# Kernel tuning notes

Hardware: AMD Instinct MI355X
Metric: run time of the kernel (lower is better)

The kernel has to match this reference:

```python
import jax, jax.numpy as jnp
import numpy as np

MASK_VALUE = -10000000.0


def setup_inputs() -> dict:
    key = jax.random.key(0)
    ks = jax.random.split(key, 8)
    U, I, J, C, E = 128, 256, 512, 128, 128
    return {
        "target_items_context": jax.random.normal(ks[0], (U, I, C), jnp.float32),
        "interacted_items_context": jax.random.normal(ks[1], (U, J, C), jnp.float32),
        "user_embeds": jax.random.normal(ks[2], (U, E), jnp.float32),
        "attention_mask": jax.random.randint(ks[3], (U, J), 0, 2) > 0,
        "w_dense": jax.random.normal(ks[4], (2 * C,), jnp.float32) * 0.02,
        "b_dense": jax.random.normal(ks[5], (1,), jnp.float32) * 0.02,
        "W_mlp": jax.random.normal(ks[6], (E + C, C), jnp.float32) * 0.02,
        "b_mlp": jax.random.normal(ks[7], (C,), jnp.float32) * 0.02,
    }


def reference(target_items_context, interacted_items_context, user_embeds,
              attention_mask, w_dense, b_dense, W_mlp, b_mlp):
    C = target_items_context.shape[-1]
    E = user_embeds.shape[-1]
    # additive attention score: tanh([t; k] @ w + b) = tanh(t@w1 + k@w2 + b)
    # (dropout is identity in eval mode)
    s_t = jnp.einsum('uic,c->ui', target_items_context, w_dense[:C])      # (U, I)
    s_k = jnp.einsum('ujc,c->uj', interacted_items_context, w_dense[C:])  # (U, J)
    scores = jnp.tanh(s_t[:, :, None] + s_k[:, None, :] + b_dense[0])     # (U, I, J)
    scores = scores + (~attention_mask)[:, None, :].astype(scores.dtype) * MASK_VALUE
    attn = jax.nn.softmax(scores, axis=-1)                                # (U, I, J)
    # weighted pooling of interacted contexts
    pooled = jnp.einsum('uij,ujc->uic', attn, interacted_items_context)   # (U, I, C)
    # mlp: relu([user; pooled] @ W + b) = relu(user@W[:E] + pooled@W[E:] + b)
    u_part = user_embeds @ W_mlp[:E]                                      # (U, C)
    user_context = jax.nn.relu(u_part[:, None, :] + pooled @ W_mlp[E:] + b_mlp)
    return user_context, attn
```

## Files before the change

kernel.cpp:

```cpp
#include <hip/hip_runtime.h>

#define UU 128
#define II 256
#define JJ 512
#define CC 128
#define EE 128
#define IB 16
#define NIB 16
#define JT 64
#define NJT 8
#define VTP 72

typedef short bf16x8 __attribute__((ext_vector_type(8)));
typedef float f32x4 __attribute__((ext_vector_type(4)));

union FragU { bf16x8 v; unsigned u[4]; };

__device__ __forceinline__ float fast_tanh(float x) {
    float ex = __expf(2.0f * x);
    return 1.0f - 2.0f / (ex + 1.0f);
}

__device__ __forceinline__ unsigned pack_bf16x2(float lo, float hi) {
    unsigned ul = __float_as_uint(lo), uh = __float_as_uint(hi);
    ul = (ul + 0x7FFFu + ((ul >> 16) & 1u)) >> 16;
    uh = (uh + 0x7FFFu + ((uh >> 16) & 1u)) >> 16;
    return ul | (uh << 16);
}

__device__ __forceinline__ short bf16s(float f) {
    unsigned u = __float_as_uint(f);
    u = (u + 0x7FFFu + ((u >> 16) & 1u)) >> 16;
    return (short)u;
}

__device__ __forceinline__ float wave_reduce_add(float v) {
#pragma unroll
    for (int k = 32; k >= 1; k >>= 1) v += __shfl_xor(v, k, 64);
    return v;
}

#define VT_BLOCKS (UU * NJT)
#define UP_BLOCKS (UU * CC / 256)

__global__ void precompute_kernel(const float* __restrict__ itc,
                                  const float* __restrict__ user,
                                  const float* __restrict__ wd,
                                  const float* __restrict__ Wm,
                                  const float* __restrict__ bm,
                                  float* __restrict__ sk_g,
                                  float* __restrict__ up_g,
                                  short* __restrict__ vtg,
                                  short* __restrict__ wtg) {
    __shared__ float vt_f[JT][CC + 4];
    int b = blockIdx.x;
    int t = threadIdx.x;
    if (b < VT_BLOCKS) {
        int u = b & 127, jt = b >> 7;
        const float* src = itc + ((size_t)u * JJ + jt * JT) * CC;
#pragma unroll
        for (int k = 0; k < 8; ++k) {
            int f = t + 256 * k;
            int row = f >> 5, c4 = (f & 31) * 4;
            *(float4*)&vt_f[row][c4] = *(const float4*)&src[(size_t)row * CC + c4];
        }
        __syncthreads();
        {
            int r = t >> 2, q4 = t & 3;
            float s = 0.f;
#pragma unroll
            for (int cc = 0; cc < 32; cc += 4) {
                float4 a = *(const float4*)&vt_f[r][q4 * 32 + cc];
                float4 w = *(const float4*)&wd[CC + q4 * 32 + cc];
                s += a.x * w.x + a.y * w.y + a.z * w.z + a.w * w.w;
            }
            s += __shfl_xor(s, 1, 64);
            s += __shfl_xor(s, 2, 64);
            if (q4 == 0) sk_g[u * JJ + jt * JT + r] = s;
        }
        {
            int c = t & 127, half = t >> 7;
            unsigned* dst = (unsigned*)(vtg + (size_t)(u * NJT + jt) * 8192) +
                            half * 2048 + c * 16;
#pragma unroll
            for (int m = 0; m < 16; ++m) {
                dst[m] = pack_bf16x2(vt_f[32 * half + 2 * m][c],
                                     vt_f[32 * half + 2 * m + 1][c]);
            }
        }
    } else if (b < VT_BLOCKS + UP_BLOCKS) {
        int idx = (b - VT_BLOCKS) * 256 + t;
        int u = idx >> 7, c = idx & 127;
        float acc = bm[c];
#pragma unroll 8
        for (int e = 0; e < EE; ++e) acc += user[u * EE + e] * Wm[e * CC + c];
        up_g[idx] = acc;
    } else {
        int n = t & 127, khalf = t >> 7;
#pragma unroll
        for (int ks2 = 0; ks2 < 2; ++ks2) {
            int ks = khalf * 2 + ks2;
#pragma unroll
            for (int g = 0; g < 4; ++g) {
                unsigned q[4];
#pragma unroll
                for (int pr = 0; pr < 4; ++pr) {
                    float lo = Wm[(size_t)(EE + 32 * ks + 8 * g + 2 * pr) * CC + n];
                    float hi = Wm[(size_t)(EE + 32 * ks + 8 * g + 2 * pr + 1) * CC + n];
                    q[pr] = pack_bf16x2(lo, hi);
                }
                *(uint4*)&wtg[ks * 4096 + n * 32 + 8 * g] =
                    make_uint4(q[0], q[1], q[2], q[3]);
            }
        }
    }
}

__global__ __launch_bounds__(256, 4) void fused_main(
    const float* __restrict__ tgt, const int* __restrict__ mask,
    const float* __restrict__ wd, const float* __restrict__ bd,
    const float* __restrict__ sk_g, const float* __restrict__ up_g,
    const short* __restrict__ vt_g, const short* __restrict__ wt_g,
    float* __restrict__ out_ctx, float* __restrict__ out_attn) {
    __shared__ __align__(16) short ps[8192];
    __shared__ __align__(16) short pooled_bf[2048];
    __shared__ float dinv_lds[IB];

    int b = blockIdx.x;
    int x = b & 7, qq = b >> 3;
    int u = x + 8 * (qq >> 4);
    int ib = qq & 15;
    int i0 = ib * IB;
    int t = threadIdx.x;
    int w = t >> 6, l = t & 63, ln = l & 15, g = l >> 4;
    int r = t >> 4, s4 = t & 15;

    float sv;
    {
        const float* trow = tgt + ((size_t)(u * II + i0 + r)) * CC + s4 * 8;
        float4 t0 = *(const float4*)&trow[0];
        float4 t1 = *(const float4*)&trow[4];
        float4 w0 = *(const float4*)&wd[s4 * 8];
        float4 w1 = *(const float4*)&wd[s4 * 8 + 4];
        float part = t0.x * w0.x + t0.y * w0.y + t0.z * w0.z + t0.w * w0.w +
                     t1.x * w1.x + t1.y * w1.y + t1.z * w1.z + t1.w * w1.w;
        part += __shfl_xor(part, 1, 64);
        part += __shfl_xor(part, 2, 64);
        part += __shfl_xor(part, 4, 64);
        part += __shfl_xor(part, 8, 64);
        sv = part + bd[0];
    }

    const float* skb = sk_g + u * JJ;
    const int* mkb = mask + u * JJ;
    unsigned pk[16];
    float rowsum = 0.f;
#pragma unroll
    for (int h = 0; h < 4; ++h) {
        int jb = 8 * (s4 + 16 * h);
        float4 k0 = *(const float4*)&skb[jb];
        float4 k1 = *(const float4*)&skb[jb + 4];
        int4 m0 = *(const int4*)&mkb[jb];
        int4 m1 = *(const int4*)&mkb[jb + 4];
        float p0 = m0.x ? __expf(fast_tanh(sv + k0.x)) : 0.f;
        float p1 = m0.y ? __expf(fast_tanh(sv + k0.y)) : 0.f;
        float p2 = m0.z ? __expf(fast_tanh(sv + k0.z)) : 0.f;
        float p3 = m0.w ? __expf(fast_tanh(sv + k0.w)) : 0.f;
        float p4 = m1.x ? __expf(fast_tanh(sv + k1.x)) : 0.f;
        float p5 = m1.y ? __expf(fast_tanh(sv + k1.y)) : 0.f;
        float p6 = m1.z ? __expf(fast_tanh(sv + k1.z)) : 0.f;
        float p7 = m1.w ? __expf(fast_tanh(sv + k1.w)) : 0.f;
        rowsum += p0 + p1 + p2 + p3 + p4 + p5 + p6 + p7;
        unsigned q0 = pack_bf16x2(p0, p1);
        unsigned q1 = pack_bf16x2(p2, p3);
        unsigned q2 = pack_bf16x2(p4, p5);
        unsigned q3 = pack_bf16x2(p6, p7);
        pk[4 * h + 0] = q0; pk[4 * h + 1] = q1;
        pk[4 * h + 2] = q2; pk[4 * h + 3] = q3;
        int gp = (s4 + 16 * h) ^ (r & 7);
        *(uint4*)((char*)ps + r * 1024 + 16 * gp) = make_uint4(q0, q1, q2, q3);
    }
    rowsum += __shfl_xor(rowsum, 1, 64);
    rowsum += __shfl_xor(rowsum, 2, 64);
    rowsum += __shfl_xor(rowsum, 4, 64);
    rowsum += __shfl_xor(rowsum, 8, 64);
    float dinv = 1.0f / rowsum;
    if (s4 == 0) dinv_lds[r] = dinv;

    const short* b_base =
        vt_g + (size_t)u * (NJT * 8192) + (32 * w + ln) * 32 + 8 * g;
    bf16x8 pb0[8], pb1[8];
#pragma unroll
    for (int s = 0; s < 8; ++s) {
        int off = (s >> 1) * 8192 + (s & 1) * 4096;
        pb0[s] = *(const bf16x8*)&b_base[off];
        pb1[s] = *(const bf16x8*)&b_base[off + 512];
    }

    {
        float* ab = out_attn + ((size_t)(u * II + i0 + r)) * JJ;
#pragma unroll
        for (int h = 0; h < 4; ++h) {
            int jb = 8 * (s4 + 16 * h);
            unsigned q0 = pk[4 * h], q1 = pk[4 * h + 1];
            unsigned q2 = pk[4 * h + 2], q3 = pk[4 * h + 3];
            f32x4 v0, v1;
            v0[0] = __uint_as_float(q0 << 16) * dinv;
            v0[1] = __uint_as_float(q0 & 0xFFFF0000u) * dinv;
            v0[2] = __uint_as_float(q1 << 16) * dinv;
            v0[3] = __uint_as_float(q1 & 0xFFFF0000u) * dinv;
            v1[0] = __uint_as_float(q2 << 16) * dinv;
            v1[1] = __uint_as_float(q2 & 0xFFFF0000u) * dinv;
            v1[2] = __uint_as_float(q3 << 16) * dinv;
            v1[3] = __uint_as_float(q3 & 0xFFFF0000u) * dinv;
            __builtin_nontemporal_store(v0, (f32x4*)&ab[jb]);
            __builtin_nontemporal_store(v1, (f32x4*)&ab[jb + 4]);
        }
    }

    asm volatile("s_waitcnt lgkmcnt(0)" ::: "memory");
    __builtin_amdgcn_s_barrier();
    asm volatile("" ::: "memory");

    f32x4 acc0 = {0.f, 0.f, 0.f, 0.f};
    f32x4 acc1 = {0.f, 0.f, 0.f, 0.f};
#pragma unroll
    for (int s = 0; s < 16; ++s) {
        bf16x8 af = *(const bf16x8*)((const char*)ps + ln * 1024 +
                                     16 * ((4 * s + g) ^ (ln & 7)));
        acc0 = __builtin_amdgcn_mfma_f32_16x16x32_bf16(af, pb0[s & 7], acc0, 0, 0, 0);
        acc1 = __builtin_amdgcn_mfma_f32_16x16x32_bf16(af, pb1[s & 7], acc1, 0, 0, 0);
        if (s < 8) {
            int off = ((s + 8) >> 1) * 8192 + ((s + 8) & 1) * 4096;
            pb0[s & 7] = *(const bf16x8*)&b_base[off];
            pb1[s & 7] = *(const bf16x8*)&b_base[off + 512];
        }
    }

    const short* wbase = wt_g + (32 * w + ln) * 32 + 8 * g;
    bf16x8 wb0[4], wb1[4];
#pragma unroll
    for (int ks = 0; ks < 4; ++ks) {
        wb0[ks] = *(const bf16x8*)&wbase[ks * 4096];
        wb1[ks] = *(const bf16x8*)&wbase[ks * 4096 + 512];
    }

#pragma unroll
    for (int ri = 0; ri < 4; ++ri) {
        int row = 4 * g + ri;
        float dv = dinv_lds[row];
        int c0 = 32 * w + ln;
        int by0 = row * 256 + 16 * ((c0 >> 3) ^ (row & 7)) + 2 * (ln & 7);
        *(short*)((char*)pooled_bf + by0) = bf16s(acc0[ri] * dv);
        int c1 = c0 + 16;
        int by1 = row * 256 + 16 * ((c1 >> 3) ^ (row & 7)) + 2 * (ln & 7);
        *(short*)((char*)pooled_bf + by1) = bf16s(acc1[ri] * dv);
    }
    asm volatile("s_waitcnt lgkmcnt(0)" ::: "memory");
    __builtin_amdgcn_s_barrier();
    asm volatile("" ::: "memory");

    f32x4 oa0 = {0.f, 0.f, 0.f, 0.f};
    f32x4 oa1 = {0.f, 0.f, 0.f, 0.f};
#pragma unroll
    for (int ks = 0; ks < 4; ++ks) {
        bf16x8 pa = *(const bf16x8*)((const char*)pooled_bf + ln * 256 +
                                     16 * ((4 * ks + g) ^ (ln & 7)));
        oa0 = __builtin_amdgcn_mfma_f32_16x16x32_bf16(pa, wb0[ks], oa0, 0, 0, 0);
        oa1 = __builtin_amdgcn_mfma_f32_16x16x32_bf16(pa, wb1[ks], oa1, 0, 0, 0);
    }
    {
        int c0 = 32 * w + ln, c1 = c0 + 16;
        float up0v = up_g[u * CC + c0];
        float up1v = up_g[u * CC + c1];
        float* ctx = out_ctx + ((size_t)(u * II + i0)) * CC;
#pragma unroll
        for (int ri = 0; ri < 4; ++ri) {
            int row = 4 * g + ri;
            __builtin_nontemporal_store(fmaxf(oa0[ri] + up0v, 0.f),
                                        &ctx[(size_t)row * CC + c0]);
            __builtin_nontemporal_store(fmaxf(oa1[ri] + up1v, 0.f),
                                        &ctx[(size_t)row * CC + c1]);
        }
    }
}

__global__ __launch_bounds__(256, 3) void fused_fallback(
    const float* __restrict__ tgt, const float* __restrict__ itc,
    const float* __restrict__ user, const int* __restrict__ mask,
    const float* __restrict__ wd, const float* __restrict__ bd,
    const float* __restrict__ Wm, const float* __restrict__ bm,
    float* __restrict__ out_ctx, float* __restrict__ out_attn) {
    __shared__ __align__(16) short Vt[CC][VTP];
    __shared__ __align__(16) float pool[IB][CC + 4];
    __shared__ __align__(16) float skv[JJ];
    __shared__ __align__(16) float stv[IB];
    __shared__ __align__(16) float upv[CC];
    __shared__ __align__(16) float dinv_lds[IB];
    __shared__ unsigned char mk[JJ];

    int b = blockIdx.x;
    int x = b & 7, q = b >> 3;
    int u = x + 8 * (q >> 4);
    int ib = q & 15;
    int i0 = ib * IB;
    int t = threadIdx.x;

    mk[t] = (unsigned char)(mask[u * JJ + t] != 0);
    mk[t + 256] = (unsigned char)(mask[u * JJ + t + 256] != 0);

    {
        int lane = t & 63, w4 = t >> 6;
        float2 w2 = *(const float2*)&wd[CC + lane * 2];
        for (int r = w4; r < JJ; r += 4) {
            float2 a = *(const float2*)&itc[((size_t)u * JJ + r) * CC + lane * 2];
            float s = wave_reduce_add(a.x * w2.x + a.y * w2.y);
            if (lane == 0) skv[r] = s;
        }
        float2 w1 = *(const float2*)&wd[lane * 2];
        float bdv = bd[0];
        for (int r = w4; r < IB; r += 4) {
            float2 a = *(const float2*)&tgt[((size_t)u * II + i0 + r) * CC + lane * 2];
            float s = wave_reduce_add(a.x * w1.x + a.y * w1.y);
            if (lane == 0) stv[r] = s + bdv;
        }
        if (t < CC) {
            float acc = bm[t];
            for (int e = 0; e < EE; ++e) acc += user[u * EE + e] * Wm[e * CC + t];
            upv[t] = acc;
        }
    }
    __syncthreads();

    const int l = t & 63;
    const int w = t >> 6;
    const int ln = l & 15;
    const int g = l >> 4;

    bf16x8 a[16];
    float rowsum = 0.0f;
    {
        float s = stv[ln];
#pragma unroll
        for (int t16 = 0; t16 < 16; ++t16) {
            int j = 32 * t16 + 8 * g;
            float4 k0 = *(const float4*)&skv[j];
            float4 k1 = *(const float4*)&skv[j + 4];
            unsigned m0 = *(const unsigned*)&mk[j];
            unsigned m1 = *(const unsigned*)&mk[j + 4];
            float pf[8];
            pf[0] = (m0 & 0x000000FFu) ? __expf(fast_tanh(s + k0.x)) : 0.0f;
            pf[1] = (m0 & 0x0000FF00u) ? __expf(fast_tanh(s + k0.y)) : 0.0f;
            pf[2] = (m0 & 0x00FF0000u) ? __expf(fast_tanh(s + k0.z)) : 0.0f;
            pf[3] = (m0 & 0xFF000000u) ? __expf(fast_tanh(s + k0.w)) : 0.0f;
            pf[4] = (m1 & 0x000000FFu) ? __expf(fast_tanh(s + k1.x)) : 0.0f;
            pf[5] = (m1 & 0x0000FF00u) ? __expf(fast_tanh(s + k1.y)) : 0.0f;
            pf[6] = (m1 & 0x00FF0000u) ? __expf(fast_tanh(s + k1.z)) : 0.0f;
            pf[7] = (m1 & 0xFF000000u) ? __expf(fast_tanh(s + k1.w)) : 0.0f;
            rowsum += pf[0] + pf[1] + pf[2] + pf[3] + pf[4] + pf[5] + pf[6] + pf[7];
            FragU cu;
            cu.u[0] = pack_bf16x2(pf[0], pf[1]);
            cu.u[1] = pack_bf16x2(pf[2], pf[3]);
            cu.u[2] = pack_bf16x2(pf[4], pf[5]);
            cu.u[3] = pack_bf16x2(pf[6], pf[7]);
            a[t16] = cu.v;
        }
    }
    rowsum += __shfl_xor(rowsum, 16, 64);
    rowsum += __shfl_xor(rowsum, 32, 64);
    float dinv = 1.0f / rowsum;
    if (t < 16) dinv_lds[t] = dinv;

    {
        float* abase = out_attn + ((size_t)(u * II + i0 + ln)) * JJ + 8 * g;
#pragma unroll
        for (int t16 = 0; t16 < 16; ++t16) {
            FragU cu; cu.v = a[t16];
            float f0 = __uint_as_float(cu.u[0] << 16) * dinv;
            float f1 = __uint_as_float(cu.u[0] & 0xFFFF0000u) * dinv;
            float f2 = __uint_as_float(cu.u[1] << 16) * dinv;
            float f3 = __uint_as_float(cu.u[1] & 0xFFFF0000u) * dinv;
            float f4 = __uint_as_float(cu.u[2] << 16) * dinv;
            float f5 = __uint_as_float(cu.u[2] & 0xFFFF0000u) * dinv;
            float f6 = __uint_as_float(cu.u[3] << 16) * dinv;
            float f7 = __uint_as_float(cu.u[3] & 0xFFFF0000u) * dinv;
            *(float4*)&abase[32 * t16] = make_float4(f0, f1, f2, f3);
            *(float4*)&abase[32 * t16 + 4] = make_float4(f4, f5, f6, f7);
        }
    }

    f32x4 acc0 = {0.f, 0.f, 0.f, 0.f};
    f32x4 acc1 = {0.f, 0.f, 0.f, 0.f};
    const float* Vu = itc + (size_t)u * JJ * CC;
    const int cg = t & 31;
    const int jp = t >> 5;
    const int n0 = w * 32;

    for (int jt = 0; jt < 8; ++jt) {
        int j0 = jt * JT;
        __syncthreads();
#pragma unroll
        for (int it = 0; it < 4; ++it) {
            int jl = 2 * (jp + 8 * it);
            const float* r0 = &Vu[(size_t)(j0 + jl) * CC];
            const float* r1 = r0 + CC;
#pragma unroll
            for (int qv = 0; qv < 4; ++qv) {
                int c = cg + 32 * qv;
                *(unsigned*)&Vt[c][jl] = pack_bf16x2(r0[c], r1[c]);
            }
        }
        __syncthreads();
#pragma unroll
        for (int kk = 0; kk < 2; ++kk) {
            bf16x8 b0 = *(const bf16x8*)&Vt[n0 + ln][32 * kk + 8 * g];
            bf16x8 b1 = *(const bf16x8*)&Vt[n0 + 16 + ln][32 * kk + 8 * g];
            acc0 = __builtin_amdgcn_mfma_f32_16x16x32_bf16(a[2 * jt + kk], b0,
                                                           acc0, 0, 0, 0);
            acc1 = __builtin_amdgcn_mfma_f32_16x16x32_bf16(a[2 * jt + kk], b1,
                                                           acc1, 0, 0, 0);
        }
    }

    __syncthreads();
    {
        float4 dv = *(const float4*)&dinv_lds[4 * g];
        float dvr[4] = {dv.x, dv.y, dv.z, dv.w};
#pragma unroll
        for (int r = 0; r < 4; ++r) {
            pool[4 * g + r][n0 + ln] = acc0[r] * dvr[r];
            pool[4 * g + r][n0 + 16 + ln] = acc1[r] * dvr[r];
        }
    }
    __syncthreads();

    {
        int tx = t & 15, ty = t >> 4;
        float o[8];
#pragma unroll
        for (int k = 0; k < 8; ++k) o[k] = 0.f;
#pragma unroll 4
        for (int k = 0; k < CC; ++k) {
            float pk = pool[ty][k];
            float4 w0 = *(const float4*)&Wm[(size_t)(EE + k) * CC + tx * 8];
            float4 w1 = *(const float4*)&Wm[(size_t)(EE + k) * CC + tx * 8 + 4];
            o[0] += pk * w0.x; o[1] += pk * w0.y; o[2] += pk * w0.z; o[3] += pk * w0.w;
            o[4] += pk * w1.x; o[5] += pk * w1.y; o[6] += pk * w1.z; o[7] += pk * w1.w;
        }
        float4 up0 = *(const float4*)&upv[tx * 8];
        float4 up1 = *(const float4*)&upv[tx * 8 + 4];
        float4 r0, r1;
        r0.x = fmaxf(o[0] + up0.x, 0.f); r0.y = fmaxf(o[1] + up0.y, 0.f);
        r0.z = fmaxf(o[2] + up0.z, 0.f); r0.w = fmaxf(o[3] + up0.w, 0.f);
        r1.x = fmaxf(o[4] + up1.x, 0.f); r1.y = fmaxf(o[5] + up1.y, 0.f);
        r1.z = fmaxf(o[6] + up1.z, 0.f); r1.w = fmaxf(o[7] + up1.w, 0.f);
        float* ctx = out_ctx + ((size_t)(u * II + i0 + ty)) * CC + tx * 8;
        *(float4*)&ctx[0] = r0;
        *(float4*)&ctx[4] = r1;
    }
}

extern "C" void kernel_launch(void* const* d_in, const int* in_sizes, int n_in,
                              void* d_out, int out_size, void* d_ws,
                              size_t ws_size, hipStream_t stream) {
    const float* tgt  = (const float*)d_in[0];
    const float* itc  = (const float*)d_in[1];
    const float* user = (const float*)d_in[2];
    const int*   mask = (const int*)d_in[3];
    const float* wd   = (const float*)d_in[4];
    const float* bd   = (const float*)d_in[5];
    const float* Wm   = (const float*)d_in[6];
    const float* bm   = (const float*)d_in[7];
    float* out_ctx  = (float*)d_out;
    float* out_attn = out_ctx + (size_t)UU * II * CC;

    size_t scalars = (size_t)(UU * JJ + UU * CC) * sizeof(float);
    size_t vt_bytes = (size_t)UU * NJT * 8192 * sizeof(short);
    size_t wt_bytes = (size_t)16384 * sizeof(short);
    size_t need = scalars + vt_bytes + wt_bytes;
    if (ws_size >= need) {
        float* sk_g = (float*)d_ws;
        float* up_g = sk_g + UU * JJ;
        short* vt_g = (short*)((char*)d_ws + scalars);
        short* wt_g = vt_g + (size_t)UU * NJT * 8192;
        int gridA = VT_BLOCKS + UP_BLOCKS + 1;
        precompute_kernel<<<gridA, 256, 0, stream>>>(itc, user, wd, Wm, bm,
                                                     sk_g, up_g, vt_g, wt_g);
        fused_main<<<UU * NIB, 256, 0, stream>>>(tgt, mask, wd, bd, sk_g, up_g,
                                                 vt_g, wt_g, out_ctx, out_attn);
    } else {
        fused_fallback<<<UU * NIB, 256, 0, stream>>>(
            tgt, itc, user, mask, wd, bd, Wm, bm, out_ctx, out_attn);
    }
}
```

Before: 61.18 us.

## Cut register pressure for higher occupancy and add nontemporal loads and vector stores

Raises the fused_main launch-bounds occupancy hint from 4 to 6 waves. To fit that budget it stops holding the packed probabilities in registers and reloads them from LDS, and it shrinks the B-operand prefetch ring from 8 to 4 entries. It also uses nontemporal loads for streamed inputs, widens the bf16 transposed stores in the prep kernel to 128-bit, and raises wave priority around the MFMA loop. The smaller prefetch depth may expose more global-load latency, and the tighter register budget could cause spills.

Measured after the change: 58.06 us. -5.1%, faster.

```diff
diff --git a/kernel.cpp b/kernel.cpp
--- a/kernel.cpp
+++ b/kernel.cpp
@@ -62,7 +62,9 @@
         for (int k = 0; k < 8; ++k) {
             int f = t + 256 * k;
             int row = f >> 5, c4 = (f & 31) * 4;
-            *(float4*)&vt_f[row][c4] = *(const float4*)&src[(size_t)row * CC + c4];
+            f32x4 v = __builtin_nontemporal_load(
+                (const f32x4*)&src[(size_t)row * CC + c4]);
+            *(f32x4*)&vt_f[row][c4] = v;
         }
         __syncthreads();
         {
@@ -83,9 +85,15 @@
             unsigned* dst = (unsigned*)(vtg + (size_t)(u * NJT + jt) * 8192) +
                             half * 2048 + c * 16;
 #pragma unroll
-            for (int m = 0; m < 16; ++m) {
-                dst[m] = pack_bf16x2(vt_f[32 * half + 2 * m][c],
-                                     vt_f[32 * half + 2 * m + 1][c]);
+            for (int m4 = 0; m4 < 4; ++m4) {
+                unsigned q[4];
+#pragma unroll
+                for (int mm = 0; mm < 4; ++mm) {
+                    int m = 4 * m4 + mm;
+                    q[mm] = pack_bf16x2(vt_f[32 * half + 2 * m][c],
+                                        vt_f[32 * half + 2 * m + 1][c]);
+                }
+                *(uint4*)&dst[4 * m4] = make_uint4(q[0], q[1], q[2], q[3]);
             }
         }
     } else if (b < VT_BLOCKS + UP_BLOCKS) {
@@ -116,7 +124,7 @@
     }
 }
 
-__global__ __launch_bounds__(256, 4) void fused_main(
+__global__ __launch_bounds__(256, 6) void fused_main(
     const float* __restrict__ tgt, const int* __restrict__ mask,
     const float* __restrict__ wd, const float* __restrict__ bd,
     const float* __restrict__ sk_g, const float* __restrict__ up_g,
@@ -138,12 +146,12 @@
     float sv;
     {
         const float* trow = tgt + ((size_t)(u * II + i0 + r)) * CC + s4 * 8;
-        float4 t0 = *(const float4*)&trow[0];
-        float4 t1 = *(const float4*)&trow[4];
+        f32x4 t0 = __builtin_nontemporal_load((const f32x4*)&trow[0]);
+        f32x4 t1 = __builtin_nontemporal_load((const f32x4*)&trow[4]);
         float4 w0 = *(const float4*)&wd[s4 * 8];
         float4 w1 = *(const float4*)&wd[s4 * 8 + 4];
-        float part = t0.x * w0.x + t0.y * w0.y + t0.z * w0.z + t0.w * w0.w +
-                     t1.x * w1.x + t1.y * w1.y + t1.z * w1.z + t1.w * w1.w;
+        float part = t0[0] * w0.x + t0[1] * w0.y + t0[2] * w0.z + t0[3] * w0.w +
+                     t1[0] * w1.x + t1[1] * w1.y + t1[2] * w1.z + t1[3] * w1.w;
         part += __shfl_xor(part, 1, 64);
         part += __shfl_xor(part, 2, 64);
         part += __shfl_xor(part, 4, 64);
@@ -153,7 +161,6 @@
 
     const float* skb = sk_g + u * JJ;
     const int* mkb = mask + u * JJ;
-    unsigned pk[16];
     float rowsum = 0.f;
 #pragma unroll
     for (int h = 0; h < 4; ++h) {
@@ -175,8 +182,6 @@
         unsigned q1 = pack_bf16x2(p2, p3);
         unsigned q2 = pack_bf16x2(p4, p5);
         unsigned q3 = pack_bf16x2(p6, p7);
-        pk[4 * h + 0] = q0; pk[4 * h + 1] = q1;
-        pk[4 * h + 2] = q2; pk[4 * h + 3] = q3;
         int gp = (s4 + 16 * h) ^ (r & 7);
         *(uint4*)((char*)ps + r * 1024 + 16 * gp) = make_uint4(q0, q1, q2, q3);
     }
@@ -189,9 +194,9 @@
 
     const short* b_base =
         vt_g + (size_t)u * (NJT * 8192) + (32 * w + ln) * 32 + 8 * g;
-    bf16x8 pb0[8], pb1[8];
-#pragma unroll
-    for (int s = 0; s < 8; ++s) {
+    bf16x8 pb0[4], pb1[4];
+#pragma unroll
+    for (int s = 0; s < 4; ++s) {
         int off = (s >> 1) * 8192 + (s & 1) * 4096;
         pb0[s] = *(const bf16x8*)&b_base[off];
         pb1[s] = *(const bf16x8*)&b_base[off + 512];
@@ -201,18 +206,18 @@
         float* ab = out_attn + ((size_t)(u * II + i0 + r)) * JJ;
 #pragma unroll
         for (int h = 0; h < 4; ++h) {
+            int gp = (s4 + 16 * h) ^ (r & 7);
+            uint4 q = *(const uint4*)((char*)ps + r * 1024 + 16 * gp);
             int jb = 8 * (s4 + 16 * h);
-            unsigned q0 = pk[4 * h], q1 = pk[4 * h + 1];
-            unsigned q2 = pk[4 * h + 2], q3 = pk[4 * h + 3];
             f32x4 v0, v1;
-            v0[0] = __uint_as_float(q0 << 16) * dinv;
-            v0[1] = __uint_as_float(q0 & 0xFFFF0000u) * dinv;
-            v0[2] = __uint_as_float(q1 << 16) * dinv;
-            v0[3] = __uint_as_float(q1 & 0xFFFF0000u) * dinv;
-            v1[0] = __uint_as_float(q2 << 16) * dinv;
-            v1[1] = __uint_as_float(q2 & 0xFFFF0000u) * dinv;
-            v1[2] = __uint_as_float(q3 << 16) * dinv;
-            v1[3] = __uint_as_float(q3 & 0xFFFF0000u) * dinv;
+            v0[0] = __uint_as_float(q.x << 16) * dinv;
+            v0[1] = __uint_as_float(q.x & 0xFFFF0000u) * dinv;
+            v0[2] = __uint_as_float(q.y << 16) * dinv;
+            v0[3] = __uint_as_float(q.y & 0xFFFF0000u) * dinv;
+            v1[0] = __uint_as_float(q.z << 16) * dinv;
+            v1[1] = __uint_as_float(q.z & 0xFFFF0000u) * dinv;
+            v1[2] = __uint_as_float(q.w << 16) * dinv;
+            v1[3] = __uint_as_float(q.w & 0xFFFF0000u) * dinv;
             __builtin_nontemporal_store(v0, (f32x4*)&ab[jb]);
             __builtin_nontemporal_store(v1, (f32x4*)&ab[jb + 4]);
         }
@@ -224,18 +229,20 @@
 
     f32x4 acc0 = {0.f, 0.f, 0.f, 0.f};
     f32x4 acc1 = {0.f, 0.f, 0.f, 0.f};
+    __builtin_amdgcn_s_setprio(1);
 #pragma unroll
     for (int s = 0; s < 16; ++s) {
         bf16x8 af = *(const bf16x8*)((const char*)ps + ln * 1024 +
                                      16 * ((4 * s + g) ^ (ln & 7)));
-        acc0 = __builtin_amdgcn_mfma_f32_16x16x32_bf16(af, pb0[s & 7], acc0, 0, 0, 0);
-        acc1 = __builtin_amdgcn_mfma_f32_16x16x32_bf16(af, pb1[s & 7], acc1, 0, 0, 0);
-        if (s < 8) {
-            int off = ((s + 8) >> 1) * 8192 + ((s + 8) & 1) * 4096;
-            pb0[s & 7] = *(const bf16x8*)&b_base[off];
-            pb1[s & 7] = *(const bf16x8*)&b_base[off + 512];
-        }
-    }
+        acc0 = __builtin_amdgcn_mfma_f32_16x16x32_bf16(af, pb0[s & 3], acc0, 0, 0, 0);
+        acc1 = __builtin_amdgcn_mfma_f32_16x16x32_bf16(af, pb1[s & 3], acc1, 0, 0, 0);
+        if (s < 12) {
+            int off = ((s + 4) >> 1) * 8192 + ((s + 4) & 1) * 4096;
+            pb0[s & 3] = *(const bf16x8*)&b_base[off];
+            pb1[s & 3] = *(const bf16x8*)&b_base[off + 512];
+        }
+    }
+    __builtin_amdgcn_s_setprio(0);
 
     const short* wbase = wt_g + (32 * w + ln) * 32 + 8 * g;
     bf16x8 wb0[4], wb1[4];
```
